# Optimization experiments

Measured on AMD Instinct MI355X. Metric: run time of the kernel, lower is better.

The kernel has to match this reference:

```python
import jax, jax.numpy as jnp
import numpy as np

NEG_INF = -1e30  # stand-in for float('-inf'); safe under softmax


def setup_inputs() -> dict:
    key = jax.random.key(0)
    k0, k1, k2, k3 = jax.random.split(key, 4)
    B, T, C, H = 8, 2048, 1024, 64
    x = jax.random.normal(k0, (B, T, C), dtype=jnp.float32)
    Wq = jax.random.normal(k1, (C, H), dtype=jnp.float32) * (C ** -0.5)
    Wk = jax.random.normal(k2, (C, H), dtype=jnp.float32) * (C ** -0.5)
    Wv = jax.random.normal(k3, (C, H), dtype=jnp.float32) * (C ** -0.5)
    return {"x": x, "Wq": Wq, "Wk": Wk, "Wv": Wv}


def reference(x, Wq, Wk, Wv):
    # x: [B, T, C]; projections (no bias): [B, T, H]
    B, T, C = x.shape
    q = jnp.einsum('btc,ch->bth', x, Wq)
    k = jnp.einsum('btc,ch->bth', x, Wk)
    v = jnp.einsum('btc,ch->bth', x, Wv)
    # raw scores (NOTE: original applies NO 1/sqrt(head_size) scaling)
    scores = jnp.einsum('bth,bsh->bts', q, k)  # [B, T, T]
    causal = jnp.tril(jnp.ones((T, T), dtype=bool))
    scores = jnp.where(causal[None, :, :], scores, NEG_INF)
    # NOTE: original uses softmax over dim=1 (query axis), kept faithfully.
    attn = jax.nn.softmax(scores, axis=1)
    # dropout is identity in eval mode
    return jnp.einsum('bts,bsh->bth', attn, v)  # [B, T, H]
```

## Files before the change

kernel.cpp:

```cpp
#include <hip/hip_runtime.h>
#include <hip/hip_bf16.h>

#define BB 8
#define TT 2048
#define CC 1024
#define HH 64
#define NTRI 528
#define NPB (TT * HH)

typedef unsigned short ushort_t;
typedef __attribute__((ext_vector_type(8))) short bf16x8;
typedef __attribute__((ext_vector_type(4))) float f32x4;

__device__ __forceinline__ float bf2f(ushort_t u) {
    unsigned int x = ((unsigned int)u) << 16;
    return __uint_as_float(x);
}
__device__ __forceinline__ ushort_t f2bf(float f) {
    unsigned int x = __float_as_uint(f);
    unsigned int lsb = (x >> 16) & 1;
    x += 0x7fffu + lsb;
    return (ushort_t)(x >> 16);
}

__global__ __launch_bounds__(256) void wsplit_kernel(
    const float* __restrict__ Wq, const float* __restrict__ Wk,
    const float* __restrict__ Wv, ushort_t* __restrict__ wpack)
{
    int slot = blockIdx.x * 256 + threadIdx.x;
    int rec = slot >> 6, lane = slot & 63;
    int quad = lane >> 4, l15 = lane & 15;
    int part = rec >> 7;
    int r2 = rec & 127;
    int kc = r2 >> 2, nt = r2 & 3;
    const float* W = (part < 2) ? Wq : (part < 4) ? Wk : Wv;
    bool lo = (part < 4) && (part & 1);
    bf16x8 o;
    #pragma unroll
    for (int j = 0; j < 8; j++) {
        int c = kc * 32 + quad * 8 + j;
        float w = W[(size_t)c * HH + nt * 16 + l15];
        ushort_t h = f2bf(w);
        o[j] = (short)(lo ? f2bf(w - bf2f(h)) : h);
    }
    *(bf16x8*)(wpack + (size_t)rec * 512 + lane * 8) = o;
}

__global__ __launch_bounds__(256) void proj_mfma(
    const float* __restrict__ x, const ushort_t* __restrict__ wpack,
    ushort_t* __restrict__ qpk, ushort_t* __restrict__ qpl,
    ushort_t* __restrict__ kpk, ushort_t* __restrict__ kpl,
    ushort_t* __restrict__ vpk)
{
    const int tid = threadIdx.x;
    const int lane = tid & 63, wid = tid >> 6;
    const int quad = lane >> 4, l15 = lane & 15;
    const int r0 = blockIdx.x * 16;
    const int nt = wid;

    __shared__ __align__(16) ushort_t xh[2][16][72];
    __shared__ __align__(16) ushort_t xl[2][16][72];
    __shared__ __align__(16) float sC[3][16][72];

    f32x4 acc[3];
    #pragma unroll
    for (int p = 0; p < 3; p++)
        acc[p] = (f32x4){0.f, 0.f, 0.f, 0.f};

    const int srow = tid >> 4, sc4 = (tid & 15) * 4;
    const float* xrow = x + (size_t)(r0 + srow) * CC + sc4;

    float4 cur = *(const float4*)xrow;

    const size_t lb8 = (size_t)lane * 8;

    for (int bk = 0; bk < 16; bk++) {
        const int buf = bk & 1;
        {
            float vv[4] = {cur.x, cur.y, cur.z, cur.w};
            ushort4 h4, l4;
            ushort_t* hp = (ushort_t*)&h4;
            ushort_t* lp = (ushort_t*)&l4;
            #pragma unroll
            for (int j = 0; j < 4; j++) {
                ushort_t h = f2bf(vv[j]);
                hp[j] = h;
                lp[j] = f2bf(vv[j] - bf2f(h));
            }
            *(ushort4*)(&xh[buf][srow][sc4]) = h4;
            *(ushort4*)(&xl[buf][srow][sc4]) = l4;
        }
        __syncthreads();
        if (bk < 15)
            cur = *(const float4*)(xrow + (bk + 1) * 64);

        #pragma unroll
        for (int c = 0; c < 2; c++) {
            const int kc = bk * 2 + c;
            bf16x8 aH = *(const bf16x8*)(&xh[buf][l15][c * 32 + quad * 8]);
            bf16x8 aL = *(const bf16x8*)(&xl[buf][l15][c * 32 + quad * 8]);
            bf16x8 bQh = *(const bf16x8*)(wpack + (((size_t)(0 * 32 + kc) * 4 + nt) * 512) + lb8);
            bf16x8 bQl = *(const bf16x8*)(wpack + (((size_t)(1 * 32 + kc) * 4 + nt) * 512) + lb8);
            bf16x8 bKh = *(const bf16x8*)(wpack + (((size_t)(2 * 32 + kc) * 4 + nt) * 512) + lb8);
            bf16x8 bKl = *(const bf16x8*)(wpack + (((size_t)(3 * 32 + kc) * 4 + nt) * 512) + lb8);
            bf16x8 bVh = *(const bf16x8*)(wpack + (((size_t)(4 * 32 + kc) * 4 + nt) * 512) + lb8);
            acc[0] = __builtin_amdgcn_mfma_f32_16x16x32_bf16(aL, bQh, acc[0], 0, 0, 0);
            acc[0] = __builtin_amdgcn_mfma_f32_16x16x32_bf16(aH, bQl, acc[0], 0, 0, 0);
            acc[0] = __builtin_amdgcn_mfma_f32_16x16x32_bf16(aH, bQh, acc[0], 0, 0, 0);
            acc[1] = __builtin_amdgcn_mfma_f32_16x16x32_bf16(aL, bKh, acc[1], 0, 0, 0);
            acc[1] = __builtin_amdgcn_mfma_f32_16x16x32_bf16(aH, bKl, acc[1], 0, 0, 0);
            acc[1] = __builtin_amdgcn_mfma_f32_16x16x32_bf16(aH, bKh, acc[1], 0, 0, 0);
            acc[2] = __builtin_amdgcn_mfma_f32_16x16x32_bf16(aH, bVh, acc[2], 0, 0, 0);
        }
    }

    #pragma unroll
    for (int p = 0; p < 3; p++)
        #pragma unroll
        for (int r = 0; r < 4; r++)
            sC[p][quad * 4 + r][nt * 16 + l15] = acc[p][r];
    __syncthreads();

    const int b = r0 >> 11;
    const int gt = (r0 & 2047) >> 4;

    {
        const int rec = wid;
        const int p = rec >> 1, ksR = rec & 1;
        const size_t dst = (size_t)b * NPB + (((size_t)ksR * 128 + gt) * 64 + lane) * 8;
        const float* src = &sC[p][l15][ksR * 32 + quad * 8];
        f32x4 v0 = *(const f32x4*)src;
        f32x4 v1 = *(const f32x4*)(src + 4);
        bf16x8 h8, l8;
        #pragma unroll
        for (int j = 0; j < 4; j++) {
            ushort_t h = f2bf(v0[j]);
            h8[j] = (short)h;
            l8[j] = (short)f2bf(v0[j] - bf2f(h));
        }
        #pragma unroll
        for (int j = 0; j < 4; j++) {
            ushort_t h = f2bf(v1[j]);
            h8[4 + j] = (short)h;
            l8[4 + j] = (short)f2bf(v1[j] - bf2f(h));
        }
        *(bf16x8*)((p == 0 ? qpk : kpk) + dst) = h8;
        *(bf16x8*)((p == 0 ? qpl : kpl) + dst) = l8;
    }
    {
        const int scL = (r0 & 2047) >> 5;
        const int half = (r0 >> 4) & 1;
        if ((quad >> 1) == half) {
            bf16x8 o;
            #pragma unroll
            for (int j = 0; j < 8; j++)
                o[j] = (short)f2bf(sC[2][(quad & 1) * 8 + j][nt * 16 + l15]);
            *(bf16x8*)(vpk + (size_t)b * NPB + (((size_t)scL * 4 + nt) * 64 + lane) * 8) = o;
        }
    }
}

__global__ __launch_bounds__(256) void colsum_mfma(
    const ushort_t* __restrict__ qpk, const ushort_t* __restrict__ qpl,
    const ushort_t* __restrict__ kpk, const ushort_t* __restrict__ kpl,
    float* __restrict__ lsum, ushort_t* __restrict__ Ppack)
{
    const int tc = blockIdx.x, st = blockIdx.y, b = blockIdx.z;
    if (tc < st) return;
    const int tid = threadIdx.x;
    const int lane = tid & 63, wid = tid >> 6;
    const int quad = lane >> 4, l15 = lane & 15;
    const int wy = wid >> 1, wx = wid & 1;
    const int t_base = tc * 128 + wy * 64;
    const int s_base = st * 128 + wx * 64;
    if (t_base < s_base) return;
    const bool needMask = (t_base == s_base);

    __shared__ __align__(16) ushort_t sT[4][64][72];

    const size_t bq = (size_t)b * NPB;
    const size_t lb8 = (size_t)lane * 8;

    bf16x8 bH[4][2], bL[4][2];
    #pragma unroll
    for (int nt = 0; nt < 4; nt++)
        #pragma unroll
        for (int ks = 0; ks < 2; ks++) {
            const size_t off = bq + (((size_t)ks * 128 + (s_base >> 4) + nt) * 64) * 8 + lb8;
            bH[nt][ks] = *(const bf16x8*)(kpk + off);
            bL[nt][ks] = *(const bf16x8*)(kpl + off);
        }

    float cs[4] = {0.f, 0.f, 0.f, 0.f};

    #pragma unroll
    for (int mt = 0; mt < 4; mt++) {
        bf16x8 aH[2], aL[2];
        #pragma unroll
        for (int ks = 0; ks < 2; ks++) {
            const size_t off = bq + (((size_t)ks * 128 + (t_base >> 4) + mt) * 64) * 8 + lb8;
            aH[ks] = *(const bf16x8*)(qpk + off);
            aL[ks] = *(const bf16x8*)(qpl + off);
        }
        f32x4 acc[4];
        #pragma unroll
        for (int nt = 0; nt < 4; nt++)
            acc[nt] = (f32x4){0.f, 0.f, 0.f, 0.f};
        #pragma unroll
        for (int nt = 0; nt < 4; nt++)
            #pragma unroll
            for (int ks = 0; ks < 2; ks++) {
                acc[nt] = __builtin_amdgcn_mfma_f32_16x16x32_bf16(aL[ks], bH[nt][ks], acc[nt], 0, 0, 0);
                acc[nt] = __builtin_amdgcn_mfma_f32_16x16x32_bf16(aH[ks], bL[nt][ks], acc[nt], 0, 0, 0);
                acc[nt] = __builtin_amdgcn_mfma_f32_16x16x32_bf16(aH[ks], bH[nt][ks], acc[nt], 0, 0, 0);
            }
        #pragma unroll
        for (int nt = 0; nt < 4; nt++)
            #pragma unroll
            for (int r = 0; r < 4; r++) {
                float e = __expf(acc[nt][r]);
                if (needMask) {
                    int t = mt * 16 + quad * 4 + r;
                    int s = nt * 16 + l15;
                    if (t < s) e = 0.f;
                }
                cs[nt] += e;
                sT[wid][mt * 16 + quad * 4 + r][nt * 16 + l15] = f2bf(e);
            }
    }

    #pragma unroll
    for (int nt = 0; nt < 4; nt++) {
        float v = cs[nt];
        v += __shfl_xor(v, 16);
        v += __shfl_xor(v, 32);
        if (quad == 0)
            atomicAdd(lsum + (size_t)b * TT + s_base + nt * 16 + l15, v);
    }

    const int ti = t_base >> 6, si = s_base >> 6;
    ushort_t* tp = Ppack + ((size_t)b * NTRI + (size_t)(ti * (ti + 1) / 2) + si) * 4096;
    #pragma unroll
    for (int rec = 0; rec < 8; rec++) {
        const int mtP = rec >> 1, ksP = rec & 1;
        bf16x8 v8 = *(const bf16x8*)&sT[wid][mtP * 16 + l15][ksP * 32 + quad * 8];
        *(bf16x8*)(tp + (size_t)rec * 512 + lb8) = v8;
    }
}

__global__ __launch_bounds__(256) void vscale_kernel(
    const ushort_t* __restrict__ vpk, const float* __restrict__ lsum,
    ushort_t* __restrict__ vps)
{
    size_t slot = (size_t)blockIdx.x * 256 + threadIdx.x;
    int lane = (int)(slot & 63);
    int quad = lane >> 4;
    int sc_b = (int)(slot >> 8);
    int b = sc_b >> 6, sc = sc_b & 63;
    bf16x8 in = *(const bf16x8*)(vpk + slot * 8);
    const float* lp = lsum + (size_t)b * TT + sc * 32 + quad * 8;
    float4 l0 = *(const float4*)lp;
    float4 l1 = *(const float4*)(lp + 4);
    float li[8] = {l0.x, l0.y, l0.z, l0.w, l1.x, l1.y, l1.z, l1.w};
    bf16x8 o;
    #pragma unroll
    for (int j = 0; j < 8; j++)
        o[j] = (short)f2bf(bf2f((ushort_t)in[j]) / li[j]);
    *(bf16x8*)(vps + slot * 8) = o;
}

__global__ __launch_bounds__(256) void attn_pv(
    const ushort_t* __restrict__ Ppack, const ushort_t* __restrict__ vps,
    float* __restrict__ out)
{
    const int p = blockIdx.x, b = blockIdx.y;
    const int tid = threadIdx.x;
    const int lane = tid & 63, wid = tid >> 6;
    const int quad = lane >> 4, l15 = lane & 15;
    const size_t lb8 = (size_t)lane * 8;

    __shared__ __align__(16) float red[4][2048];

    const ushort_t* vb_ = vps + (size_t)b * NPB;

    #pragma unroll
    for (int half = 0; half < 2; half++) {
        const int tileI = half ? (63 - p) : p;
        const int t0 = tileI * 32;
        const int ti = t0 >> 6, trel16 = (t0 & 63) >> 4;
        const size_t triBase = ((size_t)b * NTRI + (size_t)(ti * (ti + 1) / 2)) * 4096;

        f32x4 oacc[2][4];
        #pragma unroll
        for (int mt = 0; mt < 2; mt++)
            #pragma unroll
            for (int nt = 0; nt < 4; nt++)
                oacc[mt][nt] = (f32x4){0.f, 0.f, 0.f, 0.f};

        for (int s0 = wid * 64; s0 <= t0 + 31; s0 += 256) {
            const int si = s0 >> 6;
            const ushort_t* tp = Ppack + triBase + (size_t)si * 4096;
            bf16x8 pa[2][2];
            #pragma unroll
            for (int mt = 0; mt < 2; mt++)
                #pragma unroll
                for (int ks = 0; ks < 2; ks++)
                    pa[mt][ks] = *(const bf16x8*)(tp + (size_t)((trel16 + mt) * 2 + ks) * 512 + lb8);
            #pragma unroll
            for (int ks = 0; ks < 2; ks++)
                #pragma unroll
                for (int nt = 0; nt < 4; nt++) {
                    bf16x8 vb = *(const bf16x8*)(vb_ + (((size_t)(s0 >> 5) + ks) * 4 + nt) * 512 + lb8);
                    #pragma unroll
                    for (int mt = 0; mt < 2; mt++)
                        oacc[mt][nt] = __builtin_amdgcn_mfma_f32_16x16x32_bf16(pa[mt][ks], vb, oacc[mt][nt], 0, 0, 0);
                }
        }

        __syncthreads();
        #pragma unroll
        for (int mt = 0; mt < 2; mt++)
            #pragma unroll
            for (int nt = 0; nt < 4; nt++)
                #pragma unroll
                for (int r = 0; r < 4; r++)
                    red[wid][(mt * 16 + quad * 4 + r) * 64 + nt * 16 + l15] =
                        oacc[mt][nt][r];
        __syncthreads();
        for (int e = tid; e < 2048; e += 256) {
            float s_ = red[0][e] + red[1][e] + red[2][e] + red[3][e];
            out[(size_t)(b * TT + t0 + (e >> 6)) * HH + (e & 63)] = s_;
        }
        __syncthreads();
    }
}

extern "C" void kernel_launch(void* const* d_in, const int* in_sizes, int n_in,
                              void* d_out, int out_size, void* d_ws, size_t ws_size,
                              hipStream_t stream)
{
    const float* x  = (const float*)d_in[0];
    const float* Wq = (const float*)d_in[1];
    const float* Wk = (const float*)d_in[2];
    const float* Wv = (const float*)d_in[3];
    float* out = (float*)d_out;

    const size_t N = (size_t)BB * TT * HH;
    ushort_t* qpk = (ushort_t*)d_ws;
    ushort_t* qpl = qpk + N;
    ushort_t* kpk = qpl + N;
    ushort_t* kpl = kpk + N;
    ushort_t* vpk = kpl + N;
    ushort_t* vps = vpk + N;
    float* lsum = (float*)(vps + N);
    ushort_t* wpack = (ushort_t*)(lsum + (size_t)BB * TT);
    ushort_t* Ppack = wpack + (size_t)5 * 32 * 4 * 512;

    hipMemsetAsync(lsum, 0, (size_t)BB * TT * sizeof(float), stream);
    wsplit_kernel<<<dim3(160), 256, 0, stream>>>(Wq, Wk, Wv, wpack);
    proj_mfma<<<dim3(1024), 256, 0, stream>>>(x, wpack, qpk, qpl, kpk, kpl, vpk);
    colsum_mfma<<<dim3(16, 16, BB), 256, 0, stream>>>(qpk, qpl, kpk, kpl, lsum, Ppack);
    vscale_kernel<<<dim3(512), 256, 0, stream>>>(vpk, lsum, vps);
    attn_pv<<<dim3(32, BB), 256, 0, stream>>>(Ppack, vps, out);
}
```

Measured before the change: 171.2 us.

## Enlarge projection block tile to 64 rows to reuse weight fragments

The projection kernel now processes 64 rows of x per block instead of 16, so each wave loads its Q/K/V weight fragments once and applies them to four M-tiles. This cuts global weight traffic per row by four and raises MFMA work per load. In exchange the grid shrinks from 1024 to 256 blocks, LDS use grows (about 90 KB), and register pressure rises from the 12 accumulators, which may lower occupancy on a 256-CU part.

```diff
diff --git a/kernel.cpp b/kernel.cpp
--- a/kernel.cpp
+++ b/kernel.cpp
@@ -55,29 +55,35 @@
     const int tid = threadIdx.x;
     const int lane = tid & 63, wid = tid >> 6;
     const int quad = lane >> 4, l15 = lane & 15;
-    const int r0 = blockIdx.x * 16;
+    const int r0 = blockIdx.x * 64;
     const int nt = wid;
 
-    __shared__ __align__(16) ushort_t xh[2][16][72];
-    __shared__ __align__(16) ushort_t xl[2][16][72];
-    __shared__ __align__(16) float sC[3][16][72];
-
-    f32x4 acc[3];
+    __shared__ __align__(16) ushort_t xh[2][64][72];
+    __shared__ __align__(16) ushort_t xl[2][64][72];
+    __shared__ __align__(16) float sC[3][64][72];
+
+    f32x4 acc[3][4];
     #pragma unroll
     for (int p = 0; p < 3; p++)
-        acc[p] = (f32x4){0.f, 0.f, 0.f, 0.f};
-
-    const int srow = tid >> 4, sc4 = (tid & 15) * 4;
-    const float* xrow = x + (size_t)(r0 + srow) * CC + sc4;
-
-    float4 cur = *(const float4*)xrow;
+        #pragma unroll
+        for (int mt = 0; mt < 4; mt++)
+            acc[p][mt] = (f32x4){0.f, 0.f, 0.f, 0.f};
+
+    const int srow0 = tid >> 4, sc4 = (tid & 15) * 4;
+    const float* xbase = x + (size_t)(r0 + srow0) * CC + sc4;
+
+    float4 cur[4];
+    #pragma unroll
+    for (int i = 0; i < 4; i++)
+        cur[i] = *(const float4*)(xbase + (size_t)i * 16 * CC);
 
     const size_t lb8 = (size_t)lane * 8;
 
     for (int bk = 0; bk < 16; bk++) {
         const int buf = bk & 1;
-        {
-            float vv[4] = {cur.x, cur.y, cur.z, cur.w};
+        #pragma unroll
+        for (int i = 0; i < 4; i++) {
+            float vv[4] = {cur[i].x, cur[i].y, cur[i].z, cur[i].w};
             ushort4 h4, l4;
             ushort_t* hp = (ushort_t*)&h4;
             ushort_t* lp = (ushort_t*)&l4;
@@ -87,75 +93,89 @@
                 hp[j] = h;
                 lp[j] = f2bf(vv[j] - bf2f(h));
             }
-            *(ushort4*)(&xh[buf][srow][sc4]) = h4;
-            *(ushort4*)(&xl[buf][srow][sc4]) = l4;
+            *(ushort4*)(&xh[buf][srow0 + i * 16][sc4]) = h4;
+            *(ushort4*)(&xl[buf][srow0 + i * 16][sc4]) = l4;
         }
         __syncthreads();
-        if (bk < 15)
-            cur = *(const float4*)(xrow + (bk + 1) * 64);
+        if (bk < 15) {
+            #pragma unroll
+            for (int i = 0; i < 4; i++)
+                cur[i] = *(const float4*)(xbase + (size_t)i * 16 * CC + (bk + 1) * 64);
+        }
 
         #pragma unroll
         for (int c = 0; c < 2; c++) {
             const int kc = bk * 2 + c;
-            bf16x8 aH = *(const bf16x8*)(&xh[buf][l15][c * 32 + quad * 8]);
-            bf16x8 aL = *(const bf16x8*)(&xl[buf][l15][c * 32 + quad * 8]);
             bf16x8 bQh = *(const bf16x8*)(wpack + (((size_t)(0 * 32 + kc) * 4 + nt) * 512) + lb8);
             bf16x8 bQl = *(const bf16x8*)(wpack + (((size_t)(1 * 32 + kc) * 4 + nt) * 512) + lb8);
             bf16x8 bKh = *(const bf16x8*)(wpack + (((size_t)(2 * 32 + kc) * 4 + nt) * 512) + lb8);
             bf16x8 bKl = *(const bf16x8*)(wpack + (((size_t)(3 * 32 + kc) * 4 + nt) * 512) + lb8);
             bf16x8 bVh = *(const bf16x8*)(wpack + (((size_t)(4 * 32 + kc) * 4 + nt) * 512) + lb8);
-            acc[0] = __builtin_amdgcn_mfma_f32_16x16x32_bf16(aL, bQh, acc[0], 0, 0, 0);
-            acc[0] = __builtin_amdgcn_mfma_f32_16x16x32_bf16(aH, bQl, acc[0], 0, 0, 0);
-            acc[0] = __builtin_amdgcn_mfma_f32_16x16x32_bf16(aH, bQh, acc[0], 0, 0, 0);
-            acc[1] = __builtin_amdgcn_mfma_f32_16x16x32_bf16(aL, bKh, acc[1], 0, 0, 0);
-            acc[1] = __builtin_amdgcn_mfma_f32_16x16x32_bf16(aH, bKl, acc[1], 0, 0, 0);
-            acc[1] = __builtin_amdgcn_mfma_f32_16x16x32_bf16(aH, bKh, acc[1], 0, 0, 0);
-            acc[2] = __builtin_amdgcn_mfma_f32_16x16x32_bf16(aH, bVh, acc[2], 0, 0, 0);
+            #pragma unroll
+            for (int mt = 0; mt < 4; mt++) {
+                bf16x8 aH = *(const bf16x8*)(&xh[buf][mt * 16 + l15][c * 32 + quad * 8]);
+                bf16x8 aL = *(const bf16x8*)(&xl[buf][mt * 16 + l15][c * 32 + quad * 8]);
+                acc[0][mt] = __builtin_amdgcn_mfma_f32_16x16x32_bf16(aL, bQh, acc[0][mt], 0, 0, 0);
+                acc[0][mt] = __builtin_amdgcn_mfma_f32_16x16x32_bf16(aH, bQl, acc[0][mt], 0, 0, 0);
+                acc[0][mt] = __builtin_amdgcn_mfma_f32_16x16x32_bf16(aH, bQh, acc[0][mt], 0, 0, 0);
+                acc[1][mt] = __builtin_amdgcn_mfma_f32_16x16x32_bf16(aL, bKh, acc[1][mt], 0, 0, 0);
+                acc[1][mt] = __builtin_amdgcn_mfma_f32_16x16x32_bf16(aH, bKl, acc[1][mt], 0, 0, 0);
+                acc[1][mt] = __builtin_amdgcn_mfma_f32_16x16x32_bf16(aH, bKh, acc[1][mt], 0, 0, 0);
+                acc[2][mt] = __builtin_amdgcn_mfma_f32_16x16x32_bf16(aH, bVh, acc[2][mt], 0, 0, 0);
+            }
         }
     }
 
     #pragma unroll
     for (int p = 0; p < 3; p++)
         #pragma unroll
-        for (int r = 0; r < 4; r++)
-            sC[p][quad * 4 + r][nt * 16 + l15] = acc[p][r];
+        for (int mt = 0; mt < 4; mt++)
+            #pragma unroll
+            for (int r = 0; r < 4; r++)
+                sC[p][mt * 16 + quad * 4 + r][nt * 16 + l15] = acc[p][mt][r];
     __syncthreads();
 
     const int b = r0 >> 11;
-    const int gt = (r0 & 2047) >> 4;
+    const int gt0 = (r0 & 2047) >> 4;
 
     {
-        const int rec = wid;
-        const int p = rec >> 1, ksR = rec & 1;
-        const size_t dst = (size_t)b * NPB + (((size_t)ksR * 128 + gt) * 64 + lane) * 8;
-        const float* src = &sC[p][l15][ksR * 32 + quad * 8];
-        f32x4 v0 = *(const f32x4*)src;
-        f32x4 v1 = *(const f32x4*)(src + 4);
-        bf16x8 h8, l8;
-        #pragma unroll
-        for (int j = 0; j < 4; j++) {
-            ushort_t h = f2bf(v0[j]);
-            h8[j] = (short)h;
-            l8[j] = (short)f2bf(v0[j] - bf2f(h));
-        }
-        #pragma unroll
-        for (int j = 0; j < 4; j++) {
-            ushort_t h = f2bf(v1[j]);
-            h8[4 + j] = (short)h;
-            l8[4 + j] = (short)f2bf(v1[j] - bf2f(h));
-        }
-        *(bf16x8*)((p == 0 ? qpk : kpk) + dst) = h8;
-        *(bf16x8*)((p == 0 ? qpl : kpl) + dst) = l8;
+        const int mtR = wid;
+        #pragma unroll
+        for (int p = 0; p < 2; p++)
+            #pragma unroll
+            for (int ksR = 0; ksR < 2; ksR++) {
+                const size_t dst = (size_t)b * NPB +
+                    (((size_t)ksR * 128 + gt0 + mtR) * 64 + lane) * 8;
+                const float* src = &sC[p][mtR * 16 + l15][ksR * 32 + quad * 8];
+                f32x4 v0 = *(const f32x4*)src;
+                f32x4 v1 = *(const f32x4*)(src + 4);
+                bf16x8 h8, l8;
+                #pragma unroll
+                for (int j = 0; j < 4; j++) {
+                    ushort_t h = f2bf(v0[j]);
+                    h8[j] = (short)h;
+                    l8[j] = (short)f2bf(v0[j] - bf2f(h));
+                }
+                #pragma unroll
+                for (int j = 0; j < 4; j++) {
+                    ushort_t h = f2bf(v1[j]);
+                    h8[4 + j] = (short)h;
+                    l8[4 + j] = (short)f2bf(v1[j] - bf2f(h));
+                }
+                *(bf16x8*)((p == 0 ? qpk : kpk) + dst) = h8;
+                *(bf16x8*)((p == 0 ? qpl : kpl) + dst) = l8;
+            }
     }
     {
-        const int scL = (r0 & 2047) >> 5;
-        const int half = (r0 >> 4) & 1;
-        if ((quad >> 1) == half) {
+        const int scL0 = (r0 & 2047) >> 5;
+        #pragma unroll
+        for (int sc = 0; sc < 2; sc++) {
             bf16x8 o;
             #pragma unroll
             for (int j = 0; j < 8; j++)
-                o[j] = (short)f2bf(sC[2][(quad & 1) * 8 + j][nt * 16 + l15]);
-            *(bf16x8*)(vpk + (size_t)b * NPB + (((size_t)scL * 4 + nt) * 64 + lane) * 8) = o;
+                o[j] = (short)f2bf(sC[2][sc * 32 + quad * 8 + j][nt * 16 + l15]);
+            *(bf16x8*)(vpk + (size_t)b * NPB +
+                       (((size_t)(scL0 + sc) * 4 + nt) * 64 + lane) * 8) = o;
         }
     }
 }
@@ -358,7 +378,7 @@
 
     hipMemsetAsync(lsum, 0, (size_t)BB * TT * sizeof(float), stream);
     wsplit_kernel<<<dim3(160), 256, 0, stream>>>(Wq, Wk, Wv, wpack);
-    proj_mfma<<<dim3(1024), 256, 0, stream>>>(x, wpack, qpk, qpl, kpk, kpl, vpk);
+    proj_mfma<<<dim3(256), 256, 0, stream>>>(x, wpack, qpk, qpl, kpk, kpl, vpk);
     colsum_mfma<<<dim3(16, 16, BB), 256, 0, stream>>>(qpk, qpl, kpk, kpl, lsum, Ppack);
     vscale_kernel<<<dim3(512), 256, 0, stream>>>(vpk, lsum, vps);
     attn_pv<<<dim3(32, BB), 256, 0, stream>>>(Ppack, vps, out);
```

Measured after the change: 159.2 us. 7.0% less time.

## Double rows per projection block and stage full x rows in LDS

Applied to the files above, without the earlier changes.

The projection kernel now handles 32 rows per block instead of 16. It converts the whole 32x1024 x slab into bf16 hi/lo halves in LDS up front, and each weight fragment loaded from global memory is reused across two M-tiles. This halves the grid and the repeated weight-fragment traffic through L2. In exchange it drops the double-buffered overlap of x loads with MFMA work and uses close to the full LDS budget, which limits occupancy to about one block per CU.

```diff
diff --git a/kernel.cpp b/kernel.cpp
--- a/kernel.cpp
+++ b/kernel.cpp
@@ -55,108 +55,107 @@
     const int tid = threadIdx.x;
     const int lane = tid & 63, wid = tid >> 6;
     const int quad = lane >> 4, l15 = lane & 15;
-    const int r0 = blockIdx.x * 16;
+    const int r0 = blockIdx.x * 32;
     const int nt = wid;
 
-    __shared__ __align__(16) ushort_t xh[2][16][72];
-    __shared__ __align__(16) ushort_t xl[2][16][72];
-    __shared__ __align__(16) float sC[3][16][72];
-
-    f32x4 acc[3];
+    __shared__ __align__(16) ushort_t xh[32][1032];
+    __shared__ __align__(16) ushort_t xl[32][1032];
+    __shared__ __align__(16) float sC[3 * 32 * 72];
+
+    const float* xrow_base = x + (size_t)r0 * CC;
+    #pragma unroll 4
+    for (int i = 0; i < 32; i++) {
+        float4 v = *(const float4*)(xrow_base + (size_t)i * CC + tid * 4);
+        float vv[4] = {v.x, v.y, v.z, v.w};
+        ushort4 h4, l4;
+        ushort_t* hp = (ushort_t*)&h4;
+        ushort_t* lp = (ushort_t*)&l4;
+        #pragma unroll
+        for (int j = 0; j < 4; j++) {
+            ushort_t h = f2bf(vv[j]);
+            hp[j] = h;
+            lp[j] = f2bf(vv[j] - bf2f(h));
+        }
+        *(ushort4*)(&xh[i][tid * 4]) = h4;
+        *(ushort4*)(&xl[i][tid * 4]) = l4;
+    }
+    __syncthreads();
+
+    f32x4 acc[3][2];
     #pragma unroll
     for (int p = 0; p < 3; p++)
-        acc[p] = (f32x4){0.f, 0.f, 0.f, 0.f};
-
-    const int srow = tid >> 4, sc4 = (tid & 15) * 4;
-    const float* xrow = x + (size_t)(r0 + srow) * CC + sc4;
-
-    float4 cur = *(const float4*)xrow;
+        #pragma unroll
+        for (int mt = 0; mt < 2; mt++)
+            acc[p][mt] = (f32x4){0.f, 0.f, 0.f, 0.f};
 
     const size_t lb8 = (size_t)lane * 8;
 
-    for (int bk = 0; bk < 16; bk++) {
-        const int buf = bk & 1;
-        {
-            float vv[4] = {cur.x, cur.y, cur.z, cur.w};
-            ushort4 h4, l4;
-            ushort_t* hp = (ushort_t*)&h4;
-            ushort_t* lp = (ushort_t*)&l4;
+    #pragma unroll 2
+    for (int kc = 0; kc < 32; kc++) {
+        bf16x8 bQh = *(const bf16x8*)(wpack + (((size_t)(0 * 32 + kc) * 4 + nt) * 512) + lb8);
+        bf16x8 bQl = *(const bf16x8*)(wpack + (((size_t)(1 * 32 + kc) * 4 + nt) * 512) + lb8);
+        bf16x8 bKh = *(const bf16x8*)(wpack + (((size_t)(2 * 32 + kc) * 4 + nt) * 512) + lb8);
+        bf16x8 bKl = *(const bf16x8*)(wpack + (((size_t)(3 * 32 + kc) * 4 + nt) * 512) + lb8);
+        bf16x8 bVh = *(const bf16x8*)(wpack + (((size_t)(4 * 32 + kc) * 4 + nt) * 512) + lb8);
+        #pragma unroll
+        for (int mt = 0; mt < 2; mt++) {
+            bf16x8 aH = *(const bf16x8*)(&xh[mt * 16 + l15][kc * 32 + quad * 8]);
+            bf16x8 aL = *(const bf16x8*)(&xl[mt * 16 + l15][kc * 32 + quad * 8]);
+            acc[0][mt] = __builtin_amdgcn_mfma_f32_16x16x32_bf16(aL, bQh, acc[0][mt], 0, 0, 0);
+            acc[0][mt] = __builtin_amdgcn_mfma_f32_16x16x32_bf16(aH, bQl, acc[0][mt], 0, 0, 0);
+            acc[0][mt] = __builtin_amdgcn_mfma_f32_16x16x32_bf16(aH, bQh, acc[0][mt], 0, 0, 0);
+            acc[1][mt] = __builtin_amdgcn_mfma_f32_16x16x32_bf16(aL, bKh, acc[1][mt], 0, 0, 0);
+            acc[1][mt] = __builtin_amdgcn_mfma_f32_16x16x32_bf16(aH, bKl, acc[1][mt], 0, 0, 0);
+            acc[1][mt] = __builtin_amdgcn_mfma_f32_16x16x32_bf16(aH, bKh, acc[1][mt], 0, 0, 0);
+            acc[2][mt] = __builtin_amdgcn_mfma_f32_16x16x32_bf16(aH, bVh, acc[2][mt], 0, 0, 0);
+        }
+    }
+
+    #pragma unroll
+    for (int p = 0; p < 3; p++)
+        #pragma unroll
+        for (int mt = 0; mt < 2; mt++)
+            #pragma unroll
+            for (int r = 0; r < 4; r++)
+                sC[(p * 32 + mt * 16 + quad * 4 + r) * 72 + nt * 16 + l15] = acc[p][mt][r];
+    __syncthreads();
+
+    const int b = r0 >> 11;
+    {
+        const int rec = tid >> 6;
+        const int mtR = rec >> 1, ksR = rec & 1;
+        const int gt = ((r0 & 2047) >> 4) + mtR;
+        const size_t dst = (size_t)b * NPB + (((size_t)ksR * 128 + gt) * 64 + lane) * 8;
+        #pragma unroll
+        for (int p = 0; p < 2; p++) {
+            const float* src = &sC[(p * 32 + mtR * 16 + l15) * 72 + ksR * 32 + quad * 8];
+            f32x4 v0 = *(const f32x4*)src;
+            f32x4 v1 = *(const f32x4*)(src + 4);
+            bf16x8 h8, l8;
             #pragma unroll
             for (int j = 0; j < 4; j++) {
-                ushort_t h = f2bf(vv[j]);
-                hp[j] = h;
-                lp[j] = f2bf(vv[j] - bf2f(h));
+                ushort_t h = f2bf(v0[j]);
+                h8[j] = (short)h;
+                l8[j] = (short)f2bf(v0[j] - bf2f(h));
             }
-            *(ushort4*)(&xh[buf][srow][sc4]) = h4;
-            *(ushort4*)(&xl[buf][srow][sc4]) = l4;
-        }
-        __syncthreads();
-        if (bk < 15)
-            cur = *(const float4*)(xrow + (bk + 1) * 64);
-
-        #pragma unroll
-        for (int c = 0; c < 2; c++) {
-            const int kc = bk * 2 + c;
-            bf16x8 aH = *(const bf16x8*)(&xh[buf][l15][c * 32 + quad * 8]);
-            bf16x8 aL = *(const bf16x8*)(&xl[buf][l15][c * 32 + quad * 8]);
-            bf16x8 bQh = *(const bf16x8*)(wpack + (((size_t)(0 * 32 + kc) * 4 + nt) * 512) + lb8);
-            bf16x8 bQl = *(const bf16x8*)(wpack + (((size_t)(1 * 32 + kc) * 4 + nt) * 512) + lb8);
-            bf16x8 bKh = *(const bf16x8*)(wpack + (((size_t)(2 * 32 + kc) * 4 + nt) * 512) + lb8);
-            bf16x8 bKl = *(const bf16x8*)(wpack + (((size_t)(3 * 32 + kc) * 4 + nt) * 512) + lb8);
-            bf16x8 bVh = *(const bf16x8*)(wpack + (((size_t)(4 * 32 + kc) * 4 + nt) * 512) + lb8);
-            acc[0] = __builtin_amdgcn_mfma_f32_16x16x32_bf16(aL, bQh, acc[0], 0, 0, 0);
-            acc[0] = __builtin_amdgcn_mfma_f32_16x16x32_bf16(aH, bQl, acc[0], 0, 0, 0);
-            acc[0] = __builtin_amdgcn_mfma_f32_16x16x32_bf16(aH, bQh, acc[0], 0, 0, 0);
-            acc[1] = __builtin_amdgcn_mfma_f32_16x16x32_bf16(aL, bKh, acc[1], 0, 0, 0);
-            acc[1] = __builtin_amdgcn_mfma_f32_16x16x32_bf16(aH, bKl, acc[1], 0, 0, 0);
-            acc[1] = __builtin_amdgcn_mfma_f32_16x16x32_bf16(aH, bKh, acc[1], 0, 0, 0);
-            acc[2] = __builtin_amdgcn_mfma_f32_16x16x32_bf16(aH, bVh, acc[2], 0, 0, 0);
-        }
-    }
-
-    #pragma unroll
-    for (int p = 0; p < 3; p++)
-        #pragma unroll
-        for (int r = 0; r < 4; r++)
-            sC[p][quad * 4 + r][nt * 16 + l15] = acc[p][r];
-    __syncthreads();
-
-    const int b = r0 >> 11;
-    const int gt = (r0 & 2047) >> 4;
-
+            #pragma unroll
+            for (int j = 0; j < 4; j++) {
+                ushort_t h = f2bf(v1[j]);
+                h8[4 + j] = (short)h;
+                l8[4 + j] = (short)f2bf(v1[j] - bf2f(h));
+            }
+            *(bf16x8*)((p == 0 ? qpk : kpk) + dst) = h8;
+            *(bf16x8*)((p == 0 ? qpl : kpl) + dst) = l8;
+        }
+    }
     {
-        const int rec = wid;
-        const int p = rec >> 1, ksR = rec & 1;
-        const size_t dst = (size_t)b * NPB + (((size_t)ksR * 128 + gt) * 64 + lane) * 8;
-        const float* src = &sC[p][l15][ksR * 32 + quad * 8];
-        f32x4 v0 = *(const f32x4*)src;
-        f32x4 v1 = *(const f32x4*)(src + 4);
-        bf16x8 h8, l8;
-        #pragma unroll
-        for (int j = 0; j < 4; j++) {
-            ushort_t h = f2bf(v0[j]);
-            h8[j] = (short)h;
-            l8[j] = (short)f2bf(v0[j] - bf2f(h));
-        }
-        #pragma unroll
-        for (int j = 0; j < 4; j++) {
-            ushort_t h = f2bf(v1[j]);
-            h8[4 + j] = (short)h;
-            l8[4 + j] = (short)f2bf(v1[j] - bf2f(h));
-        }
-        *(bf16x8*)((p == 0 ? qpk : kpk) + dst) = h8;
-        *(bf16x8*)((p == 0 ? qpl : kpl) + dst) = l8;
-    }
-    {
+        const int ntv = tid >> 6;
         const int scL = (r0 & 2047) >> 5;
-        const int half = (r0 >> 4) & 1;
-        if ((quad >> 1) == half) {
-            bf16x8 o;
-            #pragma unroll
-            for (int j = 0; j < 8; j++)
-                o[j] = (short)f2bf(sC[2][(quad & 1) * 8 + j][nt * 16 + l15]);
-            *(bf16x8*)(vpk + (size_t)b * NPB + (((size_t)scL * 4 + nt) * 64 + lane) * 8) = o;
-        }
+        bf16x8 o;
+        #pragma unroll
+        for (int j = 0; j < 8; j++)
+            o[j] = (short)f2bf(sC[(2 * 32 + quad * 8 + j) * 72 + ntv * 16 + l15]);
+        *(bf16x8*)(vpk + (size_t)b * NPB + (((size_t)scL * 4 + ntv) * 64 + lane) * 8) = o;
     }
 }
 
@@ -358,7 +357,7 @@
 
     hipMemsetAsync(lsum, 0, (size_t)BB * TT * sizeof(float), stream);
     wsplit_kernel<<<dim3(160), 256, 0, stream>>>(Wq, Wk, Wv, wpack);
-    proj_mfma<<<dim3(1024), 256, 0, stream>>>(x, wpack, qpk, qpl, kpk, kpl, vpk);
+    proj_mfma<<<dim3(512), 256, 0, stream>>>(x, wpack, qpk, qpl, kpk, kpl, vpk);
     colsum_mfma<<<dim3(16, 16, BB), 256, 0, stream>>>(qpk, qpl, kpk, kpl, lsum, Ppack);
     vscale_kernel<<<dim3(512), 256, 0, stream>>>(vpk, lsum, vps);
     attn_pv<<<dim3(32, BB), 256, 0, stream>>>(Ppack, vps, out);
```

Result: slower. 182.7 us (+6.7%).
